# Kernel tuning notes

Measured on AMD Instinct MI355X. Metric: run time of the kernel, lower is better.

Reference implementation:

```python
import jax, jax.numpy as jnp
import numpy as np

_BN_EPS = 1e-5
_BN_SCALE = 1.0 / np.sqrt(1.0 + _BN_EPS)  # eval-mode BN with running_mean=0, running_var=1


def _bn(x, g, b):
    # eval-mode BatchNorm1d over channel dim (last axis here)
    return x * (g * _BN_SCALE) + b


def _sa_layer(src_xyz, dst_xyz, cur_i, idx, empty, p_w, p_g, p_b, m_w, m_g, m_b):
    # src_xyz: (N,3), dst_xyz: (M,3), cur_i: (N,D), idx: (M,S) int, empty: (M,) bool
    idx = idx.astype(jnp.int32)
    sp = src_xyz[idx]                       # (M,S,3) neighbor gather
    dp = dst_xyz[:, None, :]                # (M,1,3)
    feat6 = jnp.concatenate([sp - dp, jnp.broadcast_to(dp, sp.shape)], axis=-1)  # (M,S,6)
    off = jax.nn.silu(_bn(jnp.einsum('msc,dc->msd', feat6, p_w), p_g, p_b))      # (M,S,D)
    x = off + cur_i[idx]                    # (M,S,D)
    x = jnp.where(empty[:, None, None], 0.0, x)
    h = jax.nn.relu(_bn(jnp.einsum('msd,hd->msh', x, m_w), m_g, m_b))            # (M,S,H)
    return jnp.max(h, axis=1)               # (M,H) max-pool over neighbors


def reference(src_xyz, src_feats, dst_xyz, idx0, idx1, empty0, empty1,
              fc0_w, fc0_b, p0_w, p0_g, p0_b, m0_w, m0_g, m0_b,
              fc1_w, fc1_b, p1_w, p1_g, p1_b, m1_w, m1_g, m1_b,
              out_w, out_g, out_b):
    cur0 = src_feats @ fc0_w.T + fc0_b      # (N,64) fc_i of layer 0
    cur1 = src_feats @ fc1_w.T + fc1_b      # (N,64) fc_i of layer 1
    f0 = _sa_layer(src_xyz, dst_xyz, cur0, idx0, empty0, p0_w, p0_g, p0_b, m0_w, m0_g, m0_b)
    f1 = _sa_layer(src_xyz, dst_xyz, cur1, idx1, empty1, p1_w, p1_g, p1_b, m1_w, m1_g, m1_b)
    feats = jnp.concatenate([f0, f1], axis=1)                                    # (M,256)
    out = jax.nn.relu(_bn(feats @ out_w.T, out_g, out_b))                        # out_conv (1x1 conv)
    return out                               # (M,256)


def setup_inputs() -> dict:
    key = jax.random.key(0)
    ks = jax.random.split(key, 24)
    N, M, Cin, D, H, S0, S1 = 65536, 16384, 64, 64, 128, 16, 32
    inp = {
        'src_xyz': jax.random.normal(ks[0], (N, 3), jnp.float32) * 20.0,
        'src_feats': jax.random.normal(ks[1], (N, Cin), jnp.float32),
        'dst_xyz': jax.random.normal(ks[2], (M, 3), jnp.float32) * 20.0,
        'idx0': jax.random.randint(ks[3], (M, S0), 0, N, jnp.int32),
        'idx1': jax.random.randint(ks[4], (M, S1), 0, N, jnp.int32),
        'empty0': jax.random.bernoulli(ks[5], 0.05, (M,)),
        'empty1': jax.random.bernoulli(ks[6], 0.05, (M,)),
        'fc0_w': jax.random.normal(ks[7], (D, Cin), jnp.float32) / np.sqrt(Cin),
        'fc0_b': jnp.zeros((D,), jnp.float32),
        'p0_w': jax.random.normal(ks[8], (D, 6), jnp.float32) / np.sqrt(6.0),
        'p0_g': jnp.ones((D,), jnp.float32),
        'p0_b': jnp.zeros((D,), jnp.float32),
        'm0_w': jax.random.normal(ks[9], (H, D), jnp.float32) / np.sqrt(D),
        'm0_g': jnp.ones((H,), jnp.float32),
        'm0_b': jnp.zeros((H,), jnp.float32),
        'fc1_w': jax.random.normal(ks[10], (D, Cin), jnp.float32) / np.sqrt(Cin),
        'fc1_b': jnp.zeros((D,), jnp.float32),
        'p1_w': jax.random.normal(ks[11], (D, 6), jnp.float32) / np.sqrt(6.0),
        'p1_g': jnp.ones((D,), jnp.float32),
        'p1_b': jnp.zeros((D,), jnp.float32),
        'm1_w': jax.random.normal(ks[12], (H, D), jnp.float32) / np.sqrt(D),
        'm1_g': jnp.ones((H,), jnp.float32),
        'm1_b': jnp.zeros((H,), jnp.float32),
        'out_w': jax.random.normal(ks[13], (256, 2 * H), jnp.float32) / np.sqrt(2.0 * H),
        'out_g': jnp.ones((256,), jnp.float32),
        'out_b': jnp.zeros((256,), jnp.float32),
    }
    return inp
```

## Files before the change

kernel.cpp:

```cpp
#include <hip/hip_runtime.h>
#include <hip/hip_bf16.h>

typedef unsigned short ushort_t;
typedef unsigned int uint_t;
typedef __attribute__((ext_vector_type(8))) short v8s;
typedef __attribute__((ext_vector_type(4))) float v4f;

#define BN_SCALE 0.9999950000374997f

__device__ __forceinline__ float bf2f(ushort_t u) {
    union { uint_t i; float f; } v;
    v.i = ((uint_t)u) << 16;
    return v.f;
}
__device__ __forceinline__ ushort_t f2bf(float f) {
    union { uint_t i; float f; } v;
    v.f = f;
    uint_t b = v.i;
    b += 0x7fffu + ((b >> 16) & 1u);
    return (ushort_t)(b >> 16);
}

__device__ __forceinline__ v8s cvt8(const float* __restrict__ p) {
    v8s f;
    #pragma unroll
    for (int j = 0; j < 8; ++j) f[j] = (short)f2bf(p[j]);
    return f;
}

__global__ __launch_bounds__(256) void fcconv_kernel(
    const float* __restrict__ fc0_w, ushort_t* __restrict__ fc0_wb,
    const float* __restrict__ fc1_w, ushort_t* __restrict__ fc1_wb)
{
    const int b = blockIdx.x;
    const float* src = (b < 4) ? fc0_w : fc1_w;
    ushort_t*    dst = (b < 4) ? fc0_wb : fc1_wb;
    const int i = ((b & 3) * 256 + threadIdx.x) * 4;
    const v4f v = *(const v4f*)(src + i);
    ushort_t r0 = f2bf(v[0]), r1 = f2bf(v[1]), r2 = f2bf(v[2]), r3 = f2bf(v[3]);
    uint_t lo = (uint_t)r0 | ((uint_t)r1 << 16);
    uint_t hi = (uint_t)r2 | ((uint_t)r3 << 16);
    *(uint2*)(dst + i) = make_uint2(lo, hi);
}

__global__ __launch_bounds__(256) void cur_conv_kernel(
    const float* __restrict__ src_feats,
    const ushort_t* __restrict__ fc0_wb, const float* __restrict__ fc0_b,
    const ushort_t* __restrict__ fc1_wb, const float* __restrict__ fc1_b,
    ushort_t* __restrict__ cur0, ushort_t* __restrict__ cur1,
    const float* __restrict__ out_w, ushort_t* __restrict__ out_wb,
    const float* __restrict__ m0_w,  ushort_t* __restrict__ m0_wb,
    const float* __restrict__ m1_w,  ushort_t* __restrict__ m1_wb,
    const int CURB)
{
    if (blockIdx.x >= CURB) {
        const int b = blockIdx.x - CURB;
        const float* src;
        ushort_t* dst;
        int base;
        if (b < 64)      { src = out_w; dst = out_wb; base = b; }
        else if (b < 72) { src = m0_w;  dst = m0_wb;  base = b - 64; }
        else             { src = m1_w;  dst = m1_wb;  base = b - 72; }
        const int i = (base * 256 + threadIdx.x) * 4;
        const v4f v = *(const v4f*)(src + i);
        ushort_t r0 = f2bf(v[0]), r1 = f2bf(v[1]), r2 = f2bf(v[2]), r3 = f2bf(v[3]);
        uint_t lo = (uint_t)r0 | ((uint_t)r1 << 16);
        uint_t hi = (uint_t)r2 | ((uint_t)r3 << 16);
        *(uint2*)(dst + i) = make_uint2(lo, hi);
        return;
    }

    const int tid  = threadIdx.x;
    const int lane = tid & 63;
    const int wid  = tid >> 6;
    const int col  = lane & 15;
    const int quad = lane >> 4;
    const int row0 = blockIdx.x * 128 + wid * 16;

    v8s bfrag[8][2];
    float bias[8];
    #pragma unroll
    for (int ct = 0; ct < 8; ++ct) {
        const int d = (ct & 3) * 16 + col;
        const ushort_t* w = (ct < 4 ? fc0_wb : fc1_wb) + d * 64;
        bias[ct] = (ct < 4 ? fc0_b : fc1_b)[d];
        #pragma unroll
        for (int kf = 0; kf < 2; ++kf)
            bfrag[ct][kf] = *(const v8s*)(w + kf * 32 + quad * 8);
    }

    #pragma unroll
    for (int g = 0; g < 2; ++g) {
        const int rows = row0 + g * 64;

        v8s afrag[2];
        #pragma unroll
        for (int kf = 0; kf < 2; ++kf)
            afrag[kf] = cvt8(src_feats + (size_t)(rows + col) * 64 + kf * 32 + quad * 8);

        v4f acc[8];
        #pragma unroll
        for (int ct = 0; ct < 8; ++ct)
            acc[ct] = (v4f){bias[ct], bias[ct], bias[ct], bias[ct]};

        #pragma unroll
        for (int kf = 0; kf < 2; ++kf)
            #pragma unroll
            for (int ct = 0; ct < 8; ++ct)
                acc[ct] = __builtin_amdgcn_mfma_f32_16x16x32_bf16(
                    afrag[kf], bfrag[ct][kf], acc[ct], 0, 0, 0);

        #pragma unroll
        for (int ct = 0; ct < 8; ++ct) {
            ushort_t* dst = (ct < 4) ? cur0 : cur1;
            const int d = (ct & 3) * 16 + col;
            #pragma unroll
            for (int r = 0; r < 4; ++r) {
                const int n = rows + quad * 4 + r;
                dst[(size_t)n * 64 + d] = f2bf(acc[ct][r]);
            }
        }
    }
}

template <int S>
__device__ __forceinline__ void sa_body(
    const int bid,
    const float* __restrict__ src_xyz,
    const float* __restrict__ dst_xyz,
    const int*   __restrict__ idx,
    const int*   __restrict__ empty,
    const float* __restrict__ p_w,
    const float* __restrict__ p_g,
    const float* __restrict__ p_b,
    const ushort_t* __restrict__ m_wb,
    const float* __restrict__ m_g,
    const float* __restrict__ m_b,
    const ushort_t* __restrict__ cur,
    ushort_t*    __restrict__ f01,
    const int layer_off,
    ushort_t* xlds,
    v4f*      flds)
{
    constexpr int PAIRS = 128;
    constexpr int MB = PAIRS / S;
    constexpr int XP = 72;
    constexpr int T  = S / 4;

    const int tid  = threadIdx.x;
    const int lane = tid & 63;
    const int wid  = tid >> 6;
    const int m0   = bid * MB;

    {
        const int p  = tid >> 1;
        const int hf = tid & 1;
        const int m  = m0 + p / S;
        const int i  = idx[(size_t)m * S + (p & (S - 1))];
        const uint_t* crow = (const uint_t*)(cur + (size_t)i * 64) + hf * 16;
        const uint4 c0 = *(const uint4*)(crow + 0);
        const uint4 c1 = *(const uint4*)(crow + 4);
        const uint4 c2 = *(const uint4*)(crow + 8);
        const uint4 c3 = *(const uint4*)(crow + 12);
        uint_t* drow = (uint_t*)(xlds + p * XP) + hf * 16;
        *(uint4*)(drow + 0)  = c0;
        *(uint4*)(drow + 4)  = c1;
        *(uint4*)(drow + 8)  = c2;
        *(uint4*)(drow + 12) = c3;
    }
    if (tid < PAIRS) {
        const int p = tid;
        const int m = m0 + p / S;
        const int i = idx[(size_t)m * S + (p & (S - 1))];
        const float dx = dst_xyz[m * 3 + 0];
        const float dy = dst_xyz[m * 3 + 1];
        const float dz = dst_xyz[m * 3 + 2];
        v4f r;
        r[0] = src_xyz[i * 3 + 0] - dx;
        r[1] = src_xyz[i * 3 + 1] - dy;
        r[2] = src_xyz[i * 3 + 2] - dz;
        r[3] = 0.0f;
        flds[p] = r;
    }

    const int dd = (lane & 31) * 2;
    const int psub = lane >> 5;
    const float pgA = p_g[dd] * BN_SCALE;
    const float pgB = p_g[dd + 1] * BN_SCALE;
    const float pbA = p_b[dd];
    const float pbB = p_b[dd + 1];
    const float pwA0 = p_w[dd * 6 + 0] * pgA;
    const float pwA1 = p_w[dd * 6 + 1] * pgA;
    const float pwA2 = p_w[dd * 6 + 2] * pgA;
    const float pdA0 = p_w[dd * 6 + 3] * pgA;
    const float pdA1 = p_w[dd * 6 + 4] * pgA;
    const float pdA2 = p_w[dd * 6 + 5] * pgA;
    const float pwB0 = p_w[dd * 6 + 6] * pgB;
    const float pwB1 = p_w[dd * 6 + 7] * pgB;
    const float pwB2 = p_w[dd * 6 + 8] * pgB;
    const float pdB0 = p_w[dd * 6 + 9] * pgB;
    const float pdB1 = p_w[dd * 6 + 10] * pgB;
    const float pdB2 = p_w[dd * 6 + 11] * pgB;

    __syncthreads();

    const int tbase = wid * T;
    #pragma unroll
    for (int mi = 0; mi < MB; ++mi) {
        const int m = m0 + mi;
        const float dx = dst_xyz[m * 3 + 0];
        const float dy = dst_xyz[m * 3 + 1];
        const float dz = dst_xyz[m * 3 + 2];
        const int   em = empty[m];
        const float vbA = fmaf(pdA0, dx, fmaf(pdA1, dy, fmaf(pdA2, dz, pbA)));
        const float vbB = fmaf(pdB0, dx, fmaf(pdB1, dy, fmaf(pdB2, dz, pbB)));

        #pragma unroll
        for (int it = 0; it < T / 2; ++it) {
            const int p = mi * S + tbase + it * 2 + psub;
            const v4f r = flds[p];
            const uint_t cu = *(const uint_t*)(xlds + p * XP + dd);
            const float c0 = __uint_as_float(cu << 16);
            const float c1 = __uint_as_float(cu & 0xffff0000u);

            const float v0 = fmaf(pwA0, r[0], fmaf(pwA1, r[1], fmaf(pwA2, r[2], vbA)));
            const float v1 = fmaf(pwB0, r[0], fmaf(pwB1, r[1], fmaf(pwB2, r[2], vbB)));
            const float rc0 = __builtin_amdgcn_rcpf(1.0f + __expf(-v0));
            const float rc1 = __builtin_amdgcn_rcpf(1.0f + __expf(-v1));
            float x0 = fmaf(v0, rc0, c0);
            float x1 = fmaf(v1, rc1, c1);
            x0 = em ? 0.0f : x0;
            x1 = em ? 0.0f : x1;

            float2 f2; f2.x = x0; f2.y = x1;
            union { __hip_bfloat162 h2; uint_t u; } pk;
            pk.h2 = __float22bfloat162_rn(f2);
            *(uint_t*)(xlds + p * XP + dd) = pk.u;
        }
    }

    const int col  = lane & 15;
    const int quad = lane >> 4;
    v8s bfrag[2][2];
    float mgv[2], mbv[2];
    #pragma unroll
    for (int c = 0; c < 2; ++c) {
        const int h = (wid * 2 + c) * 16 + col;
        #pragma unroll
        for (int kf = 0; kf < 2; ++kf)
            bfrag[c][kf] = *(const v8s*)(m_wb + h * 64 + kf * 32 + quad * 8);
        mgv[c] = m_g[h] * BN_SCALE;
        mbv[c] = m_b[h];
    }

    __syncthreads();

    #pragma unroll
    for (int mi = 0; mi < MB; ++mi) {
        const int m = m0 + mi;
        v4f acc[S / 16][2];
        #pragma unroll
        for (int rt = 0; rt < S / 16; ++rt)
            #pragma unroll
            for (int c = 0; c < 2; ++c)
                acc[rt][c] = (v4f)0.0f;

        #pragma unroll
        for (int rt = 0; rt < S / 16; ++rt) {
            #pragma unroll
            for (int kf = 0; kf < 2; ++kf) {
                const v8s afrag = *(const v8s*)(
                    xlds + ((mi * S + rt * 16 + col)) * XP + kf * 32 + quad * 8);
                acc[rt][0] = __builtin_amdgcn_mfma_f32_16x16x32_bf16(
                    afrag, bfrag[0][kf], acc[rt][0], 0, 0, 0);
                acc[rt][1] = __builtin_amdgcn_mfma_f32_16x16x32_bf16(
                    afrag, bfrag[1][kf], acc[rt][1], 0, 0, 0);
            }
        }

        float vmax0 = 0.0f, vmax1 = 0.0f;
        #pragma unroll
        for (int c = 0; c < 2; ++c) {
            float vm = 0.0f;
            #pragma unroll
            for (int rt = 0; rt < S / 16; ++rt)
                #pragma unroll
                for (int r = 0; r < 4; ++r) {
                    const float y = fmaf(acc[rt][c][r], mgv[c], mbv[c]);
                    vm = fmaxf(vm, y);
                }
            vm = fmaxf(vm, __shfl_xor(vm, 16));
            vm = fmaxf(vm, __shfl_xor(vm, 32));
            if (c == 0) vmax0 = vm; else vmax1 = vm;
        }
        if (lane < 32) {
            const int c = lane >> 4;
            const float val = (c == 0) ? vmax0 : vmax1;
            f01[m * 256 + layer_off + (wid * 2 + c) * 16 + (lane & 15)] = f2bf(val);
        }
    }
}

__global__ __launch_bounds__(256, 6) void sa_fused_kernel(
    const float* __restrict__ src_xyz, const float* __restrict__ dst_xyz,
    const int* __restrict__ idx0, const int* __restrict__ empty0,
    const float* __restrict__ p0_w, const float* __restrict__ p0_g, const float* __restrict__ p0_b,
    const ushort_t* __restrict__ m0_wb, const float* __restrict__ m0_g, const float* __restrict__ m0_b,
    const ushort_t* __restrict__ cur0,
    const int* __restrict__ idx1, const int* __restrict__ empty1,
    const float* __restrict__ p1_w, const float* __restrict__ p1_g, const float* __restrict__ p1_b,
    const ushort_t* __restrict__ m1_wb, const float* __restrict__ m1_g, const float* __restrict__ m1_b,
    const ushort_t* __restrict__ cur1,
    ushort_t* __restrict__ f01, const int G32)
{
    __shared__ __align__(16) ushort_t xlds[128 * 72];
    __shared__ v4f      flds[128];

    const int b = blockIdx.x;
    if (b < G32)
        sa_body<32>(b, src_xyz, dst_xyz, idx1, empty1, p1_w, p1_g, p1_b,
                    m1_wb, m1_g, m1_b, cur1, f01, 128, xlds, flds);
    else
        sa_body<16>(b - G32, src_xyz, dst_xyz, idx0, empty0, p0_w, p0_g, p0_b,
                    m0_wb, m0_g, m0_b, cur0, f01, 0, xlds, flds);
}

__global__ __launch_bounds__(256) void out_kernel(
    const ushort_t* __restrict__ f01,
    const ushort_t* __restrict__ out_wb,
    const float*    __restrict__ out_g,
    const float*    __restrict__ out_b,
    float*          __restrict__ out)
{
    const int tid  = threadIdx.x;
    const int lane = tid & 63;
    const int wid  = tid >> 6;
    const int col  = lane & 15;
    const int quad = lane >> 4;
    const int m0   = blockIdx.x * 32;

    v8s afrag[2][8];
    #pragma unroll
    for (int rg = 0; rg < 2; ++rg)
        #pragma unroll
        for (int kf = 0; kf < 8; ++kf)
            afrag[rg][kf] = *(const v8s*)(
                f01 + (size_t)(m0 + rg * 16 + col) * 256 + kf * 32 + quad * 8);

    v4f acc[2][4];
    #pragma unroll
    for (int rg = 0; rg < 2; ++rg)
        #pragma unroll
        for (int c = 0; c < 4; ++c) acc[rg][c] = (v4f)0.0f;

    #pragma unroll
    for (int kf = 0; kf < 8; ++kf) {
        #pragma unroll
        for (int c = 0; c < 4; ++c) {
            const int n = (wid * 4 + c) * 16 + col;
            const v8s b = *(const v8s*)(out_wb + (size_t)n * 256 + kf * 32 + quad * 8);
            acc[0][c] = __builtin_amdgcn_mfma_f32_16x16x32_bf16(afrag[0][kf], b, acc[0][c], 0, 0, 0);
            acc[1][c] = __builtin_amdgcn_mfma_f32_16x16x32_bf16(afrag[1][kf], b, acc[1][c], 0, 0, 0);
        }
    }

    #pragma unroll
    for (int c = 0; c < 4; ++c) {
        const int n  = (wid * 4 + c) * 16 + col;
        const float og = out_g[n] * BN_SCALE;
        const float ob = out_b[n];
        #pragma unroll
        for (int rg = 0; rg < 2; ++rg)
            #pragma unroll
            for (int r = 0; r < 4; ++r) {
                float y = fmaf(acc[rg][c][r], og, ob);
                y = fmaxf(y, 0.0f);
                out[(size_t)(m0 + rg * 16 + quad * 4 + r) * 256 + n] = y;
            }
    }
}

extern "C" void kernel_launch(void* const* d_in, const int* in_sizes, int n_in,
                              void* d_out, int out_size, void* d_ws, size_t ws_size,
                              hipStream_t stream)
{
    const float* src_xyz   = (const float*)d_in[0];
    const float* src_feats = (const float*)d_in[1];
    const float* dst_xyz   = (const float*)d_in[2];
    const int*   idx0      = (const int*)d_in[3];
    const int*   idx1      = (const int*)d_in[4];
    const int*   empty0    = (const int*)d_in[5];
    const int*   empty1    = (const int*)d_in[6];
    const float* fc0_w     = (const float*)d_in[7];
    const float* fc0_b     = (const float*)d_in[8];
    const float* p0_w      = (const float*)d_in[9];
    const float* p0_g      = (const float*)d_in[10];
    const float* p0_b      = (const float*)d_in[11];
    const float* m0_w      = (const float*)d_in[12];
    const float* m0_g      = (const float*)d_in[13];
    const float* m0_b      = (const float*)d_in[14];
    const float* fc1_w     = (const float*)d_in[15];
    const float* fc1_b     = (const float*)d_in[16];
    const float* p1_w      = (const float*)d_in[17];
    const float* p1_g      = (const float*)d_in[18];
    const float* p1_b      = (const float*)d_in[19];
    const float* m1_w      = (const float*)d_in[20];
    const float* m1_g      = (const float*)d_in[21];
    const float* m1_b      = (const float*)d_in[22];
    const float* out_w     = (const float*)d_in[23];
    const float* out_g     = (const float*)d_in[24];
    const float* out_b     = (const float*)d_in[25];

    const int N = in_sizes[0] / 3;
    const int M = in_sizes[2] / 3;

    ushort_t* cur0   = (ushort_t*)d_ws;
    ushort_t* cur1   = cur0 + (size_t)N * 64;
    ushort_t* f01    = cur1 + (size_t)N * 64;
    ushort_t* out_wb = f01 + (size_t)M * 256;
    ushort_t* m0_wb  = out_wb + 256 * 256;
    ushort_t* m1_wb  = m0_wb + 128 * 64;
    ushort_t* fc0_wb = m1_wb + 128 * 64;
    ushort_t* fc1_wb = fc0_wb + 64 * 64;

    const int G32 = M / 4;
    const int G16 = M / 8;
    const int CURB = N / 128;

    fcconv_kernel<<<8, 256, 0, stream>>>(fc0_w, fc0_wb, fc1_w, fc1_wb);
    cur_conv_kernel<<<CURB + 80, 256, 0, stream>>>(
        src_feats, fc0_wb, fc0_b, fc1_wb, fc1_b, cur0, cur1,
        out_w, out_wb, m0_w, m0_wb, m1_w, m1_wb, CURB);
    sa_fused_kernel<<<G32 + G16, 256, 0, stream>>>(
        src_xyz, dst_xyz,
        idx0, empty0, p0_w, p0_g, p0_b, m0_wb, m0_g, m0_b, cur0,
        idx1, empty1, p1_w, p1_g, p1_b, m1_wb, m1_g, m1_b, cur1,
        f01, G32);
    out_kernel<<<M / 32, 256, 0, stream>>>(f01, out_wb, out_g, out_b,
                                           (float*)d_out);
}
```

Measured before the change: 180.0 us.

## Swap MFMA operands for vectorized row-contiguous stores and skip empty centers

New measurement: 182.5 us. No clear change (+1.4%).

```diff
diff --git a/kernel.cpp b/kernel.cpp
--- a/kernel.cpp
+++ b/kernel.cpp
@@ -8,11 +8,6 @@
 
 #define BN_SCALE 0.9999950000374997f
 
-__device__ __forceinline__ float bf2f(ushort_t u) {
-    union { uint_t i; float f; } v;
-    v.i = ((uint_t)u) << 16;
-    return v.f;
-}
 __device__ __forceinline__ ushort_t f2bf(float f) {
     union { uint_t i; float f; } v;
     v.f = f;
@@ -21,11 +16,20 @@
     return (ushort_t)(b >> 16);
 }
 
-__device__ __forceinline__ v8s cvt8(const float* __restrict__ p) {
-    v8s f;
-    #pragma unroll
-    for (int j = 0; j < 8; ++j) f[j] = (short)f2bf(p[j]);
-    return f;
+__device__ __forceinline__ uint_t pkbf(float a, float b) {
+    union { __hip_bfloat162 h2; uint_t u; } t;
+    float2 f; f.x = a; f.y = b;
+    t.h2 = __float22bfloat162_rn(f);
+    return t.u;
+}
+
+__device__ __forceinline__ v8s cvt8f(const float* __restrict__ p) {
+    const v4f a = *(const v4f*)p;
+    const v4f b = *(const v4f*)(p + 4);
+    union { uint4 q; v8s s; } r;
+    r.q = make_uint4(pkbf(a[0], a[1]), pkbf(a[2], a[3]),
+                     pkbf(b[0], b[1]), pkbf(b[2], b[3]));
+    return r.s;
 }
 
 __global__ __launch_bounds__(256) void fcconv_kernel(
@@ -37,10 +41,7 @@
     ushort_t*    dst = (b < 4) ? fc0_wb : fc1_wb;
     const int i = ((b & 3) * 256 + threadIdx.x) * 4;
     const v4f v = *(const v4f*)(src + i);
-    ushort_t r0 = f2bf(v[0]), r1 = f2bf(v[1]), r2 = f2bf(v[2]), r3 = f2bf(v[3]);
-    uint_t lo = (uint_t)r0 | ((uint_t)r1 << 16);
-    uint_t hi = (uint_t)r2 | ((uint_t)r3 << 16);
-    *(uint2*)(dst + i) = make_uint2(lo, hi);
+    *(uint2*)(dst + i) = make_uint2(pkbf(v[0], v[1]), pkbf(v[2], v[3]));
 }
 
 __global__ __launch_bounds__(256) void cur_conv_kernel(
@@ -63,10 +64,7 @@
         else             { src = m1_w;  dst = m1_wb;  base = b - 72; }
         const int i = (base * 256 + threadIdx.x) * 4;
         const v4f v = *(const v4f*)(src + i);
-        ushort_t r0 = f2bf(v[0]), r1 = f2bf(v[1]), r2 = f2bf(v[2]), r3 = f2bf(v[3]);
-        uint_t lo = (uint_t)r0 | ((uint_t)r1 << 16);
-        uint_t hi = (uint_t)r2 | ((uint_t)r3 << 16);
-        *(uint2*)(dst + i) = make_uint2(lo, hi);
+        *(uint2*)(dst + i) = make_uint2(pkbf(v[0], v[1]), pkbf(v[2], v[3]));
         return;
     }
 
@@ -78,12 +76,12 @@
     const int row0 = blockIdx.x * 128 + wid * 16;
 
     v8s bfrag[8][2];
-    float bias[8];
+    v4f bias4[8];
     #pragma unroll
     for (int ct = 0; ct < 8; ++ct) {
         const int d = (ct & 3) * 16 + col;
         const ushort_t* w = (ct < 4 ? fc0_wb : fc1_wb) + d * 64;
-        bias[ct] = (ct < 4 ? fc0_b : fc1_b)[d];
+        bias4[ct] = *(const v4f*)((ct < 4 ? fc0_b : fc1_b) + (ct & 3) * 16 + quad * 4);
         #pragma unroll
         for (int kf = 0; kf < 2; ++kf)
             bfrag[ct][kf] = *(const v8s*)(w + kf * 32 + quad * 8);
@@ -92,33 +90,31 @@
     #pragma unroll
     for (int g = 0; g < 2; ++g) {
         const int rows = row0 + g * 64;
+        const int n    = rows + col;
 
         v8s afrag[2];
         #pragma unroll
         for (int kf = 0; kf < 2; ++kf)
-            afrag[kf] = cvt8(src_feats + (size_t)(rows + col) * 64 + kf * 32 + quad * 8);
+            afrag[kf] = cvt8f(src_feats + (size_t)n * 64 + kf * 32 + quad * 8);
 
         v4f acc[8];
         #pragma unroll
         for (int ct = 0; ct < 8; ++ct)
-            acc[ct] = (v4f){bias[ct], bias[ct], bias[ct], bias[ct]};
+            acc[ct] = bias4[ct];
 
         #pragma unroll
         for (int kf = 0; kf < 2; ++kf)
             #pragma unroll
             for (int ct = 0; ct < 8; ++ct)
                 acc[ct] = __builtin_amdgcn_mfma_f32_16x16x32_bf16(
-                    afrag[kf], bfrag[ct][kf], acc[ct], 0, 0, 0);
+                    bfrag[ct][kf], afrag[kf], acc[ct], 0, 0, 0);
 
         #pragma unroll
         for (int ct = 0; ct < 8; ++ct) {
             ushort_t* dst = (ct < 4) ? cur0 : cur1;
-            const int d = (ct & 3) * 16 + col;
-            #pragma unroll
-            for (int r = 0; r < 4; ++r) {
-                const int n = rows + quad * 4 + r;
-                dst[(size_t)n * 64 + d] = f2bf(acc[ct][r]);
-            }
+            const uint2 u = make_uint2(pkbf(acc[ct][0], acc[ct][1]),
+                                       pkbf(acc[ct][2], acc[ct][3]));
+            *(uint2*)(dst + (size_t)n * 64 + (ct & 3) * 16 + quad * 4) = u;
         }
     }
 }
@@ -208,34 +204,37 @@
     #pragma unroll
     for (int mi = 0; mi < MB; ++mi) {
         const int m = m0 + mi;
-        const float dx = dst_xyz[m * 3 + 0];
-        const float dy = dst_xyz[m * 3 + 1];
-        const float dz = dst_xyz[m * 3 + 2];
-        const int   em = empty[m];
-        const float vbA = fmaf(pdA0, dx, fmaf(pdA1, dy, fmaf(pdA2, dz, pbA)));
-        const float vbB = fmaf(pdB0, dx, fmaf(pdB1, dy, fmaf(pdB2, dz, pbB)));
-
-        #pragma unroll
-        for (int it = 0; it < T / 2; ++it) {
-            const int p = mi * S + tbase + it * 2 + psub;
-            const v4f r = flds[p];
-            const uint_t cu = *(const uint_t*)(xlds + p * XP + dd);
-            const float c0 = __uint_as_float(cu << 16);
-            const float c1 = __uint_as_float(cu & 0xffff0000u);
-
-            const float v0 = fmaf(pwA0, r[0], fmaf(pwA1, r[1], fmaf(pwA2, r[2], vbA)));
-            const float v1 = fmaf(pwB0, r[0], fmaf(pwB1, r[1], fmaf(pwB2, r[2], vbB)));
-            const float rc0 = __builtin_amdgcn_rcpf(1.0f + __expf(-v0));
-            const float rc1 = __builtin_amdgcn_rcpf(1.0f + __expf(-v1));
-            float x0 = fmaf(v0, rc0, c0);
-            float x1 = fmaf(v1, rc1, c1);
-            x0 = em ? 0.0f : x0;
-            x1 = em ? 0.0f : x1;
-
-            float2 f2; f2.x = x0; f2.y = x1;
-            union { __hip_bfloat162 h2; uint_t u; } pk;
-            pk.h2 = __float22bfloat162_rn(f2);
-            *(uint_t*)(xlds + p * XP + dd) = pk.u;
+        const int em = empty[m];
+        if (em) {
+            #pragma unroll
+            for (int it = 0; it < T / 2; ++it) {
+                const int p = mi * S + tbase + it * 2 + psub;
+                *(uint_t*)(xlds + p * XP + dd) = 0u;
+            }
+        } else {
+            const float dx = dst_xyz[m * 3 + 0];
+            const float dy = dst_xyz[m * 3 + 1];
+            const float dz = dst_xyz[m * 3 + 2];
+            const float vbA = fmaf(pdA0, dx, fmaf(pdA1, dy, fmaf(pdA2, dz, pbA)));
+            const float vbB = fmaf(pdB0, dx, fmaf(pdB1, dy, fmaf(pdB2, dz, pbB)));
+
+            #pragma unroll
+            for (int it = 0; it < T / 2; ++it) {
+                const int p = mi * S + tbase + it * 2 + psub;
+                const v4f r = flds[p];
+                const uint_t cu = *(const uint_t*)(xlds + p * XP + dd);
+                const float c0 = __uint_as_float(cu << 16);
+                const float c1 = __uint_as_float(cu & 0xffff0000u);
+
+                const float v0 = fmaf(pwA0, r[0], fmaf(pwA1, r[1], fmaf(pwA2, r[2], vbA)));
+                const float v1 = fmaf(pwB0, r[0], fmaf(pwB1, r[1], fmaf(pwB2, r[2], vbB)));
+                const float rc0 = __builtin_amdgcn_rcpf(1.0f + __expf(-v0));
+                const float rc1 = __builtin_amdgcn_rcpf(1.0f + __expf(-v1));
+                const float x0 = fmaf(v0, rc0, c0);
+                const float x1 = fmaf(v1, rc1, c1);
+
+                *(uint_t*)(xlds + p * XP + dd) = pkbf(x0, x1);
+            }
         }
     }
 
@@ -359,24 +358,24 @@
         for (int c = 0; c < 4; ++c) {
             const int n = (wid * 4 + c) * 16 + col;
             const v8s b = *(const v8s*)(out_wb + (size_t)n * 256 + kf * 32 + quad * 8);
-            acc[0][c] = __builtin_amdgcn_mfma_f32_16x16x32_bf16(afrag[0][kf], b, acc[0][c], 0, 0, 0);
-            acc[1][c] = __builtin_amdgcn_mfma_f32_16x16x32_bf16(afrag[1][kf], b, acc[1][c], 0, 0, 0);
+            acc[0][c] = __builtin_amdgcn_mfma_f32_16x16x32_bf16(b, afrag[0][kf], acc[0][c], 0, 0, 0);
+            acc[1][c] = __builtin_amdgcn_mfma_f32_16x16x32_bf16(b, afrag[1][kf], acc[1][c], 0, 0, 0);
         }
     }
 
     #pragma unroll
     for (int c = 0; c < 4; ++c) {
-        const int n  = (wid * 4 + c) * 16 + col;
-        const float og = out_g[n] * BN_SCALE;
-        const float ob = out_b[n];
-        #pragma unroll
-        for (int rg = 0; rg < 2; ++rg)
-            #pragma unroll
-            for (int r = 0; r < 4; ++r) {
-                float y = fmaf(acc[rg][c][r], og, ob);
-                y = fmaxf(y, 0.0f);
-                out[(size_t)(m0 + rg * 16 + quad * 4 + r) * 256 + n] = y;
-            }
+        const int nb = (wid * 4 + c) * 16 + quad * 4;
+        const v4f og4 = *(const v4f*)(out_g + nb);
+        const v4f ob4 = *(const v4f*)(out_b + nb);
+        #pragma unroll
+        for (int rg = 0; rg < 2; ++rg) {
+            v4f y;
+            #pragma unroll
+            for (int r = 0; r < 4; ++r)
+                y[r] = fmaxf(fmaf(acc[rg][c][r], og4[r] * BN_SCALE, ob4[r]), 0.0f);
+            *(v4f*)(out + (size_t)(m0 + rg * 16 + col) * 256 + nb) = y;
+        }
     }
 }
 
```
